# Optimization experiments

Hardware: AMD Instinct MI355X
Metric: run time of the kernel (lower is better)

Reference implementation:

```python
import jax, jax.numpy as jnp
import numpy as np

NUM_STATES = 3
MAX_ITERS = 20
EPS = 1e-8
STATE_PRIOR = jnp.array([0.1, 0.8, 0.1], dtype=jnp.float32)
TRANS = jnp.array([[0.98, 0.01, 0.01],
                   [0.01, 0.98, 0.01],
                   [0.01, 0.01, 0.98]], dtype=jnp.float32)

N_SPOTS = 20000
N_GENES = 3000
N_EDGES = 120000


def setup_inputs() -> dict:
    key = jax.random.key(0)
    k1, k2, k3 = jax.random.split(key, 3)
    norm_x = jax.random.uniform(k1, (N_SPOTS, N_GENES), dtype=jnp.float32)
    reconstructed_features = jax.random.uniform(k2, (N_SPOTS, N_GENES), dtype=jnp.float32)
    edge_index = jax.random.randint(k3, (2, N_EDGES), 0, N_SPOTS, dtype=jnp.int32)
    return {"norm_x": norm_x, "reconstructed_features": reconstructed_features,
            "edge_index": edge_index}


def _mcmc_state_probs(spot_mean, m, key):
    """Vectorized Metropolis-Hastings over all samples.

    spot_mean: (N,) standardized per-spot mean (detached)
    m:         (N,) raw per-spot feature means (detached)
    Faithful quirk of the original: likelihood(state, mean) indexes mean[state]
    where state in {0,1,2}, i.e. it uses the means of the FIRST num_states
    SAMPLES as the per-state gaussian centers, and sums over all spots.
    """
    # L[s] = sum_j exp(-0.5 * (spot_mean_j - m[s])^2), s = 0..NUM_STATES-1
    L = jnp.sum(jnp.exp(-0.5 * (spot_mean[None, :] - m[:NUM_STATES, None]) ** 2), axis=1)  # (3,)
    N = spot_mean.shape[0]
    k0, kloop = jax.random.split(key)
    states0 = jax.random.randint(k0, (N,), 0, NUM_STATES)

    def step(states, k):
        k1, k2 = jax.random.split(k)
        cand = jax.random.randint(k1, (N,), 0, NUM_STATES)
        prior_ratio = STATE_PRIOR[cand] / STATE_PRIOR[states]
        lik_ratio = L[cand] / L[states]
        trans_ratio = TRANS[states, cand] / TRANS[cand, states]
        acc = prior_ratio * lik_ratio * trans_ratio
        u = jax.random.uniform(k2, (N,))
        new_states = jnp.where(u < acc, cand, states)
        return new_states, jax.nn.one_hot(new_states, NUM_STATES, dtype=jnp.float32)

    keys = jax.random.split(kloop, MAX_ITERS)
    _, onehots = jax.lax.scan(step, states0, keys)  # (MAX_ITERS, N, 3)
    return jnp.sum(onehots, axis=0)  # (N, 3) visit counts = state_probs


def reference(norm_x, reconstructed_features, edge_index):
    N = reconstructed_features.shape[0]
    # per-spot mean, detached (original does .detach().cpu().numpy())
    m = jax.lax.stop_gradient(jnp.mean(reconstructed_features, axis=1))  # (N,)
    spot_mean = (m - m.mean()) / (m.std() + EPS)

    state_probs = _mcmc_state_probs(spot_mean, m, jax.random.key(42))  # (N, 3)

    # scatter_mean(state_probs[row], col) over the spatial graph
    row, col = edge_index[0], edge_index[1]
    sums = jax.ops.segment_sum(state_probs[row], col, num_segments=N)          # (N, 3)
    cnt = jax.ops.segment_sum(jnp.ones(row.shape, jnp.float32), col, num_segments=N)
    smoothed = sums / jnp.maximum(cnt, 1.0)[:, None]

    final_states = jnp.argmax(smoothed, axis=1).astype(jnp.float32) + 1.0      # (N,)

    adj = reconstructed_features * final_states[:, None]                       # (N, G)
    copy_sum = jnp.sum(adj, axis=1, keepdims=True)
    pseudo_sum = jnp.sum(norm_x, axis=1, keepdims=True)
    norm_copy = adj / (copy_sum + EPS) * pseudo_sum

    # range endpoints are detached (.item() in torch); inner min/max are not
    rmin = jax.lax.stop_gradient(norm_copy.min()) * 0.8
    rmax = jax.lax.stop_gradient(norm_copy.max()) * 1.2
    norm_copy = (norm_copy - norm_copy.min()) / (norm_copy.max() - norm_copy.min() + EPS)
    norm_copy = norm_copy * (rmax - rmin) + rmin
    norm_copy = norm_copy / jnp.mean(norm_copy)

    reg_loss = jnp.sum(reconstructed_features ** 2) * 1e-4
    return norm_copy, reg_loss
```

## Files before the change

### kernel.cpp

```cpp
#include <hip/hip_runtime.h>
#include <cmath>


static constexpr int NS = 20000;
static constexpr int NG = 3000;
static constexpr int G4 = NG / 4;
static constexpr int NW = NS / 4;
static constexpr int NB = NW / 4;
static constexpr float EPS = 1e-8f;

typedef float fv4 __attribute__((ext_vector_type(4)));


__global__ __launch_bounds__(256) void k_stats(
    const fv4* __restrict__ nx, const fv4* __restrict__ rf,
    float* __restrict__ S, float* __restrict__ P,
    float* __restrict__ PST, float* __restrict__ PSQ,
    float* __restrict__ PMN, float* __restrict__ PMX)
{
    const int wid  = threadIdx.x >> 6;
    const int lane = threadIdx.x & 63;
    const int gw   = blockIdx.x * 4 + wid;
    float st = 0.f, sq = 0.f, tmn = INFINITY, tmx = -INFINITY;
    #pragma unroll
    for (int k = 0; k < 4; ++k) {
        const int row = gw + k * NW;
        const fv4* r = rf + (size_t)row * G4;
        const fv4* n = nx + (size_t)row * G4;
        float s = 0.f, p = 0.f, q = 0.f, mn = INFINITY, mx = -INFINITY;
        for (int c = lane; c < G4; c += 64) {
            fv4 a = r[c];
            fv4 b = __builtin_nontemporal_load(n + c);
            s += (a.x + a.y) + (a.z + a.w);
            q += a.x * a.x + a.y * a.y + a.z * a.z + a.w * a.w;
            mn = fminf(mn, fminf(fminf(a.x, a.y), fminf(a.z, a.w)));
            mx = fmaxf(mx, fmaxf(fmaxf(a.x, a.y), fmaxf(a.z, a.w)));
            p += (b.x + b.y) + (b.z + b.w);
        }
        #pragma unroll
        for (int off = 32; off > 0; off >>= 1) {
            s += __shfl_down(s, off);
            p += __shfl_down(p, off);
            q += __shfl_down(q, off);
            mn = fminf(mn, __shfl_down(mn, off));
            mx = fmaxf(mx, __shfl_down(mx, off));
        }
        if (lane == 0) {
            S[row] = s; P[row] = p;
            const float sc = p / (s + EPS);
            st += sc * s;
            sq += q;
            tmn = fminf(tmn, mn * sc);
            tmx = fmaxf(tmx, mx * sc);
        }
    }
    __shared__ float lst[4], lsq[4], lmn[4], lmx[4];
    if (lane == 0) { lst[wid] = st; lsq[wid] = sq; lmn[wid] = tmn; lmx[wid] = tmx; }
    __syncthreads();
    if (threadIdx.x == 0) {
        PST[blockIdx.x] = (lst[0] + lst[1]) + (lst[2] + lst[3]);
        PSQ[blockIdx.x] = (lsq[0] + lsq[1]) + (lsq[2] + lsq[3]);
        PMN[blockIdx.x] = fminf(fminf(lmn[0], lmn[1]), fminf(lmn[2], lmn[3]));
        PMX[blockIdx.x] = fmaxf(fmaxf(lmx[0], lmx[1]), fmaxf(lmx[2], lmx[3]));
    }
}

__global__ __launch_bounds__(256) void k_scalars(
    const float* __restrict__ PST, const float* __restrict__ PSQ,
    const float* __restrict__ PMN, const float* __restrict__ PMX,
    float* __restrict__ AB, float* __restrict__ loss_out)
{
    double st = 0.0, sq = 0.0;
    float tmn = INFINITY, tmx = -INFINITY;
    for (int i = threadIdx.x; i < NB; i += 256) {
        st += (double)PST[i];
        sq += (double)PSQ[i];
        tmn = fminf(tmn, PMN[i]);
        tmx = fmaxf(tmx, PMX[i]);
    }
    #pragma unroll
    for (int off = 32; off > 0; off >>= 1) {
        st += __shfl_down(st, off);
        sq += __shfl_down(sq, off);
        tmn = fminf(tmn, __shfl_down(tmn, off));
        tmx = fmaxf(tmx, __shfl_down(tmx, off));
    }
    __shared__ double lst[4], lsq[4];
    __shared__ float lmn[4], lmx[4];
    const int wid = threadIdx.x >> 6;
    if ((threadIdx.x & 63) == 0) { lst[wid] = st; lsq[wid] = sq; lmn[wid] = tmn; lmx[wid] = tmx; }
    __syncthreads();
    if (threadIdx.x == 0) {
        st  = (lst[0] + lst[1]) + (lst[2] + lst[3]);
        sq  = (lsq[0] + lsq[1]) + (lsq[2] + lsq[3]);
        tmn = fminf(fminf(lmn[0], lmn[1]), fminf(lmn[2], lmn[3]));
        tmx = fmaxf(fmaxf(lmx[0], lmx[1]), fmaxf(lmx[2], lmx[3]));
        const float rmin = tmn * 0.8f;
        const float rmax = tmx * 1.2f;
        const float a = (rmax - rmin) / (tmx - tmn + EPS);
        const float mean_t = (float)(st / (double)((long long)NS * (long long)NG));
        const float mean_u = (mean_t - tmn) * a + rmin;
        AB[0] = a / mean_u;
        AB[1] = (rmin - tmn * a) / mean_u;
        *loss_out = (float)(sq * 1e-4);
    }
}

__global__ __launch_bounds__(256) void k_finalize(
    const fv4* __restrict__ rf,
    const float* __restrict__ S, const float* __restrict__ P,
    const float* __restrict__ AB,
    fv4* __restrict__ out)
{
    const int row  = blockIdx.x * 4 + (threadIdx.x >> 6);
    const int lane = threadIdx.x & 63;
    const float A = AB[0], B = AB[1];
    const float c = (P[row] / (S[row] + EPS)) * A;
    const fv4* r = rf + (size_t)row * G4;
    fv4* o = out + (size_t)row * G4;
    for (int i = lane; i < G4; i += 64) {
        fv4 a = r[i];
        fv4 v;
        v.x = fmaf(a.x, c, B);
        v.y = fmaf(a.y, c, B);
        v.z = fmaf(a.z, c, B);
        v.w = fmaf(a.w, c, B);
        __builtin_nontemporal_store(v, o + i);
    }
}

extern "C" void kernel_launch(void* const* d_in, const int* in_sizes, int n_in,
                              void* d_out, int out_size, void* d_ws, size_t ws_size,
                              hipStream_t stream) {
    const float* nx = (const float*)d_in[0];
    const float* rf = (const float*)d_in[1];
    float* out = (float*)d_out;
    float* ws  = (float*)d_ws;
    float* S   = ws;
    float* P   = ws + NS;
    float* PST = ws + 2 * NS;
    float* PSQ = PST + NB;
    float* PMN = PST + 2 * NB;
    float* PMX = PST + 3 * NB;
    float* AB  = PST + 4 * NB;
    float* loss_out = out + (out_size - 1);

    k_stats   <<<NB,     256, 0, stream>>>((const fv4*)nx, (const fv4*)rf,
                                           S, P, PST, PSQ, PMN, PMX);
    k_scalars <<<1,      256, 0, stream>>>(PST, PSQ, PMN, PMX, AB, loss_out);
    k_finalize<<<NS / 4, 256, 0, stream>>>((const fv4*)rf, S, P, AB, (fv4*)out);
}
```

Baseline: 151.0 us.

## Stage norm_x rows through LDS via direct global-to-LDS loads in stats kernel

The stats kernel now issues each wave's whole reconstructed-feature row into registers (12 fv4 loads) and streams the norm_x row directly into LDS with global_load_lds, then reduces both after a single vmcnt wait. The goal is more memory-level parallelism per wave, with the norm_x traffic bypassing VGPRs. In exchange it uses 48KB of LDS per block, which limits occupancy. It also unrolls the row loop only once, and a missing wait before reusing the LDS stage across iterations could race.

```diff
diff --git a/kernel.cpp b/kernel.cpp
--- a/kernel.cpp
+++ b/kernel.cpp
@@ -11,6 +11,9 @@
 
 typedef float fv4 __attribute__((ext_vector_type(4)));
 
+#define GLOBAL_AS __attribute__((address_space(1)))
+#define LDS_AS    __attribute__((address_space(3)))
+
 
 __global__ __launch_bounds__(256) void k_stats(
     const fv4* __restrict__ nx, const fv4* __restrict__ rf,
@@ -18,25 +21,62 @@
     float* __restrict__ PST, float* __restrict__ PSQ,
     float* __restrict__ PMN, float* __restrict__ PMX)
 {
+    __shared__ fv4 stage[4][768];
     const int wid  = threadIdx.x >> 6;
     const int lane = threadIdx.x & 63;
     const int gw   = blockIdx.x * 4 + wid;
     float st = 0.f, sq = 0.f, tmn = INFINITY, tmx = -INFINITY;
-    #pragma unroll
+
+    #pragma unroll 1
     for (int k = 0; k < 4; ++k) {
         const int row = gw + k * NW;
         const fv4* r = rf + (size_t)row * G4;
         const fv4* n = nx + (size_t)row * G4;
-        float s = 0.f, p = 0.f, q = 0.f, mn = INFINITY, mx = -INFINITY;
-        for (int c = lane; c < G4; c += 64) {
-            fv4 a = r[c];
-            fv4 b = __builtin_nontemporal_load(n + c);
-            s += (a.x + a.y) + (a.z + a.w);
-            q += a.x * a.x + a.y * a.y + a.z * a.z + a.w * a.w;
-            mn = fminf(mn, fminf(fminf(a.x, a.y), fminf(a.z, a.w)));
-            mx = fmaxf(mx, fmaxf(fmaxf(a.x, a.y), fmaxf(a.z, a.w)));
-            p += (b.x + b.y) + (b.z + b.w);
+
+        __builtin_amdgcn_sched_barrier(0);
+
+        fv4 a[12];
+        #pragma unroll
+        for (int i = 0; i < 12; ++i) {
+            int c = lane + i * 64;
+            if (c > G4 - 1) c = G4 - 1;
+            a[i] = r[c];
         }
+
+        #pragma unroll
+        for (int i = 0; i < 11; ++i)
+            __builtin_amdgcn_global_load_lds(
+                (const GLOBAL_AS void*)(n + lane + i * 64),
+                (LDS_AS void*)&stage[wid][i * 64], 16, 0, 2);
+        if (lane < G4 - 11 * 64)
+            __builtin_amdgcn_global_load_lds(
+                (const GLOBAL_AS void*)(n + lane + 704),
+                (LDS_AS void*)&stage[wid][704], 16, 0, 2);
+        __builtin_amdgcn_sched_barrier(0);
+
+        float s = 0.f, q = 0.f, mn = INFINITY, mx = -INFINITY;
+        #pragma unroll
+        for (int i = 0; i < 12; ++i) {
+            if (i < 11 || lane < G4 - 11 * 64) {
+                fv4 v = a[i];
+                s += (v.x + v.y) + (v.z + v.w);
+                q += v.x * v.x + v.y * v.y + v.z * v.z + v.w * v.w;
+                mn = fminf(mn, fminf(fminf(v.x, v.y), fminf(v.z, v.w)));
+                mx = fmaxf(mx, fmaxf(fmaxf(v.x, v.y), fmaxf(v.z, v.w)));
+            }
+        }
+
+        asm volatile("s_waitcnt vmcnt(0)" ::: "memory");
+        __builtin_amdgcn_sched_barrier(0);
+        float p = 0.f;
+        #pragma unroll
+        for (int i = 0; i < 12; ++i) {
+            if (i < 11 || lane < G4 - 11 * 64) {
+                fv4 b = stage[wid][lane + i * 64];
+                p += (b.x + b.y) + (b.z + b.w);
+            }
+        }
+
         #pragma unroll
         for (int off = 32; off > 0; off >>= 1) {
             s += __shfl_down(s, off);
@@ -54,6 +94,7 @@
             tmx = fmaxf(tmx, mx * sc);
         }
     }
+
     __shared__ float lst[4], lsq[4], lmn[4], lmx[4];
     if (lane == 0) { lst[wid] = st; lsq[wid] = sq; lmn[wid] = tmn; lmx[wid] = tmx; }
     __syncthreads();
```

Measured after the change: 150.3 us. No clear change (-0.4%).
